# Optimization experiments

Measured on AMD Instinct MI355X. Metric: run time of the kernel, lower is better.

The kernel has to match this reference:

```python
import jax, jax.numpy as jnp
import numpy as np


def setup_inputs() -> dict:
    key = jax.random.key(0)
    ks = jax.random.split(key, 6)
    B, S, F = 8, 2048, 1024
    scale = 1.0 / np.sqrt(F)
    return {
        "query": jax.random.normal(ks[0], (B, S, F), dtype=jnp.float32),
        "key": jax.random.normal(ks[1], (B, S, F), dtype=jnp.float32),
        "value": jax.random.normal(ks[2], (B, S, F), dtype=jnp.float32),
        "Wq": jax.random.normal(ks[3], (F, F), dtype=jnp.float32) * scale,
        "Wk": jax.random.normal(ks[4], (F, F), dtype=jnp.float32) * scale,
        "Wv": jax.random.normal(ks[5], (F, F), dtype=jnp.float32) * scale,
    }


def reference(query, key, value, Wq, Wk, Wv):
    # nn.Linear(bias=False): x @ W.T, W is [out, in]
    q_t = jnp.einsum('bsf,gf->bsg', query, Wq)
    k_t = jnp.einsum('bsf,gf->bsg', key, Wk)
    v_t = jnp.einsum('bsf,gf->bsg', value, Wv)
    F = k_t.shape[-1]
    scale = jnp.asarray(1.0, q_t.dtype) / jnp.sqrt(jnp.asarray(F, q_t.dtype))
    attn = jnp.einsum('bij,bkj->bik', q_t, k_t) * scale  # [B, S, S]
    # original uses nn.Softmax(dim=1): softmax over the query (i) axis
    attn = jax.nn.softmax(attn, axis=1)
    # 'bii,bij->bij': diagonal of attn scales rows of v_t
    diag = jnp.diagonal(attn, axis1=1, axis2=2)  # [B, S]
    proj = diag[:, :, None] * v_t  # [B, S, F]
    return proj
```

## Files before the change

kernel.cpp:

```cpp
#include <hip/hip_runtime.h>


typedef _Float16 f16x8 __attribute__((ext_vector_type(8)));
typedef float    f32x4 __attribute__((ext_vector_type(4)));

#define COLIC 8
#define SCALE 0.03125f

typedef __attribute__((address_space(1))) const unsigned int g_u32_t;
typedef __attribute__((address_space(3))) unsigned int l_u32_t;

__device__ __forceinline__ void gload16(const _Float16* g, _Float16* l) {
  __builtin_amdgcn_global_load_lds((g_u32_t*)g, (l_u32_t*)l, 16, 0, 0);
}

__device__ __forceinline__ void stage_tile64(const _Float16* gbase, int ldk,
                                             _Float16* lds, int w, int lane) {
#pragma unroll
  for (int c = 0; c < 4; ++c) {
    const int blk = c * 4 + w;
    const int o = (blk << 10) + (lane << 4);
    const int row = o >> 7;
    const int colb = (o & 127) ^ ((row & 7) << 4);
    gload16(gbase + (size_t)row * ldk + (colb >> 1), lds + (blk << 9));
  }
}

struct Conv3Args {
  const float* src[3];
  _Float16* dst[3];
};
__global__ __launch_bounds__(256)
void conv3_f32_f16(Conv3Args a, int n8) {
  const float* __restrict__ src = a.src[blockIdx.y];
  _Float16* __restrict__ dst = a.dst[blockIdx.y];
  for (int i = blockIdx.x * 256 + threadIdx.x; i < n8; i += gridDim.x * 256) {
    const float4 x = ((const float4*)src)[2 * i];
    const float4 y = ((const float4*)src)[2 * i + 1];
    f16x8 o;
    o[0] = (_Float16)x.x; o[1] = (_Float16)x.y;
    o[2] = (_Float16)x.z; o[3] = (_Float16)x.w;
    o[4] = (_Float16)y.x; o[5] = (_Float16)y.y;
    o[6] = (_Float16)y.z; o[7] = (_Float16)y.w;
    ((f16x8*)dst)[i] = o;
  }
}

template <int F16OUT>
__global__ __launch_bounds__(256)
void gemm_mfma(const _Float16* __restrict__ A, const _Float16* __restrict__ B,
               _Float16* __restrict__ C16, float* __restrict__ C32,
               const float* __restrict__ mpart, const float* __restrict__ lpart,
               const float* __restrict__ sdiag, int BSz,
               int M, int N, int Kd) {
  __shared__ __align__(16) _Float16 As[128 * 64];
  __shared__ __align__(16) _Float16 Bs[128 * 64];
  __shared__ float diagS[128];
  const int tid = threadIdx.x;
  const int w = tid >> 6, lane = tid & 63;
  const int wr = w >> 1, wc = w & 1;
  const int lr = lane & 15, kq = lane >> 4;
  const int swz = (lr & 7) << 4;
  const int bm = blockIdx.x * 128, bn = blockIdx.y * 128;

  if (!F16OUT && tid < 128) {
    const int row = bm + tid;
    float Mx = -3.0e38f;
#pragma unroll
    for (int c = 0; c < COLIC; ++c) Mx = fmaxf(Mx, mpart[(size_t)c * BSz + row]);
    float L = 0.0f;
#pragma unroll
    for (int c = 0; c < COLIC; ++c)
      L += lpart[(size_t)c * BSz + row] * __expf(mpart[(size_t)c * BSz + row] - Mx);
    diagS[tid] = __expf(sdiag[row] - Mx) / L;
  }

  f32x4 acc[4][4] = {};
  for (int k0 = 0; k0 < Kd; k0 += 64) {
    stage_tile64(A + (size_t)bm * Kd + k0, Kd, As, w, lane);
    stage_tile64(B + (size_t)bn * Kd + k0, Kd, Bs, w, lane);
    __syncthreads();
    f16x8 af[4][2], bf[4][2];
#pragma unroll
    for (int mi = 0; mi < 4; ++mi) {
      const int ro = (wr * 64 + mi * 16 + lr) << 7;
      af[mi][0] = *(const f16x8*)&As[(ro + ((kq * 16) ^ swz)) >> 1];
      af[mi][1] = *(const f16x8*)&As[(ro + ((64 + kq * 16) ^ swz)) >> 1];
    }
#pragma unroll
    for (int ni = 0; ni < 4; ++ni) {
      const int ro = (wc * 64 + ni * 16 + lr) << 7;
      bf[ni][0] = *(const f16x8*)&Bs[(ro + ((kq * 16) ^ swz)) >> 1];
      bf[ni][1] = *(const f16x8*)&Bs[(ro + ((64 + kq * 16) ^ swz)) >> 1];
    }
#pragma unroll
    for (int ks = 0; ks < 2; ++ks)
#pragma unroll
      for (int mi = 0; mi < 4; ++mi)
#pragma unroll
        for (int ni = 0; ni < 4; ++ni)
          acc[mi][ni] = __builtin_amdgcn_mfma_f32_16x16x32_f16(af[mi][ks], bf[ni][ks], acc[mi][ni], 0, 0, 0);
    __syncthreads();
  }
#pragma unroll
  for (int mi = 0; mi < 4; ++mi) {
#pragma unroll
    for (int j = 0; j < 4; ++j) {
      const int rloc = wr * 64 + mi * 16 + kq * 4 + j;
      const int row = bm + rloc;
      float s = 1.0f;
      if (!F16OUT) s = diagS[rloc];
#pragma unroll
      for (int ni = 0; ni < 4; ++ni) {
        const int col = bn + wc * 64 + ni * 16 + lr;
        if (F16OUT) C16[(size_t)row * N + col] = (_Float16)acc[mi][ni][j];
        else        C32[(size_t)row * N + col] = acc[mi][ni][j] * s;
      }
    }
  }
}

__global__ __launch_bounds__(256)
void col_stats_mfma(const _Float16* __restrict__ qt, const _Float16* __restrict__ kt,
                    float* __restrict__ mpart, float* __restrict__ lpart,
                    float* __restrict__ sdiag, int S, int Fd, int chunk) {
  __shared__ __align__(16) _Float16 Qs[128 * 64];
  __shared__ __align__(16) _Float16 Ks[128 * 64];
  __shared__ float redM[8][128];
  __shared__ float redL[8][128];
  const int b = blockIdx.z, jb = blockIdx.x, ic = blockIdx.y;
  const int j0 = jb * 128;
  const _Float16* Q = qt + (size_t)b * S * Fd;
  const _Float16* K = kt + (size_t)b * S * Fd;
  const int tid = threadIdx.x;
  const int w = tid >> 6, lane = tid & 63;
  const int wr = w >> 1, wc = w & 1;
  const int lr = lane & 15, kq = lane >> 4;
  const int swz = (lr & 7) << 4;

  float m[4], l[4];
#pragma unroll
  for (int ni = 0; ni < 4; ++ni) { m[ni] = -3.0e38f; l[ni] = 0.0f; }

  for (int it = 0; it < chunk >> 7; ++it) {
    const int i0 = ic * chunk + (it << 7);
    f32x4 acc[4][4] = {};
    for (int k0 = 0; k0 < Fd; k0 += 64) {
      stage_tile64(Q + (size_t)i0 * Fd + k0, Fd, Qs, w, lane);
      stage_tile64(K + (size_t)j0 * Fd + k0, Fd, Ks, w, lane);
      __syncthreads();
      f16x8 af[4][2], bf[4][2];
#pragma unroll
      for (int mi = 0; mi < 4; ++mi) {
        const int ro = (wr * 64 + mi * 16 + lr) << 7;
        af[mi][0] = *(const f16x8*)&Qs[(ro + ((kq * 16) ^ swz)) >> 1];
        af[mi][1] = *(const f16x8*)&Qs[(ro + ((64 + kq * 16) ^ swz)) >> 1];
      }
#pragma unroll
      for (int ni = 0; ni < 4; ++ni) {
        const int ro = (wc * 64 + ni * 16 + lr) << 7;
        bf[ni][0] = *(const f16x8*)&Ks[(ro + ((kq * 16) ^ swz)) >> 1];
        bf[ni][1] = *(const f16x8*)&Ks[(ro + ((64 + kq * 16) ^ swz)) >> 1];
      }
#pragma unroll
      for (int ks = 0; ks < 2; ++ks)
#pragma unroll
        for (int mi = 0; mi < 4; ++mi)
#pragma unroll
          for (int ni = 0; ni < 4; ++ni)
            acc[mi][ni] = __builtin_amdgcn_mfma_f32_16x16x32_f16(af[mi][ks], bf[ni][ks], acc[mi][ni], 0, 0, 0);
      __syncthreads();
    }
    if (i0 == j0 && wr == wc && (lr >> 2) == kq) {
      const int j = lr & 3;
#pragma unroll
      for (int jj = 0; jj < 4; ++jj)
        sdiag[(size_t)b * S + j0 + wc * 64 + jj * 16 + lr] = acc[jj][jj][j] * SCALE;
    }
#pragma unroll
    for (int ni = 0; ni < 4; ++ni) {
      float tm = -3.0e38f;
#pragma unroll
      for (int mi = 0; mi < 4; ++mi)
#pragma unroll
        for (int jj = 0; jj < 4; ++jj) tm = fmaxf(tm, acc[mi][ni][jj]);
      tm *= SCALE;
      const float mn = fmaxf(m[ni], tm);
      float add = 0.0f;
#pragma unroll
      for (int mi = 0; mi < 4; ++mi)
#pragma unroll
        for (int jj = 0; jj < 4; ++jj) add += __expf(acc[mi][ni][jj] * SCALE - mn);
      l[ni] = l[ni] * __expf(m[ni] - mn) + add;
      m[ni] = mn;
    }
  }
  __syncthreads();
  const int p = wr * 4 + kq;
#pragma unroll
  for (int ni = 0; ni < 4; ++ni) {
    const int col = wc * 64 + ni * 16 + lr;
    redM[p][col] = m[ni];
    redL[p][col] = l[ni];
  }
  __syncthreads();
  if (tid < 128) {
    float M = -3.0e38f;
#pragma unroll
    for (int q = 0; q < 8; ++q) M = fmaxf(M, redM[q][tid]);
    float L = 0.0f;
#pragma unroll
    for (int q = 0; q < 8; ++q) L += redL[q][tid] * __expf(redM[q][tid] - M);
    const size_t idx = ((size_t)ic * gridDim.z + b) * S + j0 + tid;
    mpart[idx] = M;
    lpart[idx] = L;
  }
}

extern "C" void kernel_launch(void* const* d_in, const int* in_sizes, int n_in,
                              void* d_out, int out_size, void* d_ws, size_t ws_size,
                              hipStream_t stream) {
  const float* query = (const float*)d_in[0];
  const float* key   = (const float*)d_in[1];
  const float* value = (const float*)d_in[2];
  const float* Wq    = (const float*)d_in[3];
  const float* Wk    = (const float*)d_in[4];
  const float* Wv    = (const float*)d_in[5];

  const int F = 1024;
  const int BS = in_sizes[0] / F;
  const int B = 8;
  const int S = BS / B;

  _Float16* q16  = (_Float16*)d_ws;
  _Float16* k16  = q16 + (size_t)BS * F;
  _Float16* v16  = k16 + (size_t)BS * F;
  _Float16* wq16 = v16 + (size_t)BS * F;
  _Float16* wk16 = wq16 + (size_t)F * F;
  _Float16* wv16 = wk16 + (size_t)F * F;
  float* mpart = (float*)(wv16 + (size_t)F * F);
  float* lpart = mpart + (size_t)COLIC * BS;
  float* sdiag = lpart + (size_t)COLIC * BS;

  _Float16* qt16 = (_Float16*)d_out;
  _Float16* kt16 = qt16 + (size_t)BS * F;

  const dim3 blk(256);
  const int n8x = BS * F / 8, n8w = F * F / 8;

  Conv3Args ax; ax.src[0] = query; ax.src[1] = key; ax.src[2] = value;
  ax.dst[0] = q16; ax.dst[1] = k16; ax.dst[2] = v16;
  conv3_f32_f16<<<dim3(2048, 3), blk, 0, stream>>>(ax, n8x);

  Conv3Args aw; aw.src[0] = Wq; aw.src[1] = Wk; aw.src[2] = Wv;
  aw.dst[0] = wq16; aw.dst[1] = wk16; aw.dst[2] = wv16;
  conv3_f32_f16<<<dim3(512, 3), blk, 0, stream>>>(aw, n8w);

  const dim3 ggrid(BS / 128, F / 128);
  gemm_mfma<1><<<ggrid, blk, 0, stream>>>(q16, wq16, qt16, (float*)nullptr,
                                          (const float*)nullptr, (const float*)nullptr,
                                          (const float*)nullptr, BS, BS, F, F);
  gemm_mfma<1><<<ggrid, blk, 0, stream>>>(k16, wk16, kt16, (float*)nullptr,
                                          (const float*)nullptr, (const float*)nullptr,
                                          (const float*)nullptr, BS, BS, F, F);

  const dim3 sgrid(S / 128, COLIC, B);
  col_stats_mfma<<<sgrid, blk, 0, stream>>>(qt16, kt16, mpart, lpart, sdiag,
                                            S, F, S / COLIC);

  gemm_mfma<0><<<ggrid, blk, 0, stream>>>(v16, wv16, (_Float16*)nullptr, (float*)d_out,
                                          mpart, lpart, sdiag, BS, BS, F, F);
}
```

Baseline: 281.8 us.

## Fold Wq and Wk into one combined weight to drop the query projection GEMM

Uses the identity q_t·k_tᵀ = query·(Wqᵀ Wk)·keyᵀ. The code transposes Wq and Wk, multiplies them once into a 1024x1024 matrix W2, then projects only the key through W2. col_stats now reads the raw fp16 query directly, which removes one of the two large projection GEMMs. It also remaps col_stats block indices so that neighbouring blocks share inputs for better cache locality. The trade-off is a small extra FxF GEMM plus a transpose kernel, and a different fp16 rounding path through the combined weight that could change accuracy.

```diff
diff --git a/kernel.cpp b/kernel.cpp
--- a/kernel.cpp
+++ b/kernel.cpp
@@ -46,6 +46,43 @@
   }
 }
 
+struct Conv2Args {
+  const float* src[2];
+  _Float16* dst[2];
+};
+__global__ __launch_bounds__(256)
+void convT_f32_f16(Conv2Args a) {
+  __shared__ float Ts[64][65];
+  const float* __restrict__ src = a.src[blockIdx.z];
+  _Float16* __restrict__ dst = a.dst[blockIdx.z];
+  const int g0 = blockIdx.x * 64, f0 = blockIdx.y * 64;
+  const int tid = threadIdx.x;
+  {
+    const int r = tid >> 4;
+    const int c4 = (tid & 15) << 2;
+#pragma unroll
+    for (int p = 0; p < 4; ++p) {
+      const int row = p * 16 + r;
+      const float4 v = *(const float4*)&src[(size_t)(g0 + row) * 1024 + f0 + c4];
+      Ts[row][c4 + 0] = v.x; Ts[row][c4 + 1] = v.y;
+      Ts[row][c4 + 2] = v.z; Ts[row][c4 + 3] = v.w;
+    }
+  }
+  __syncthreads();
+  {
+    const int f = tid >> 3;
+    const int gs = (tid & 7) << 3;
+#pragma unroll
+    for (int p = 0; p < 2; ++p) {
+      const int fr = p * 32 + f;
+      f16x8 v;
+#pragma unroll
+      for (int j = 0; j < 8; ++j) v[j] = (_Float16)Ts[gs + j][fr];
+      *(f16x8*)&dst[(size_t)(f0 + fr) * 1024 + g0 + gs] = v;
+    }
+  }
+}
+
 template <int F16OUT>
 __global__ __launch_bounds__(256)
 void gemm_mfma(const _Float16* __restrict__ A, const _Float16* __restrict__ B,
@@ -128,7 +165,11 @@
   __shared__ __align__(16) _Float16 Ks[128 * 64];
   __shared__ float redM[8][128];
   __shared__ float redL[8][128];
-  const int b = blockIdx.z, jb = blockIdx.x, ic = blockIdx.y;
+  const int t = blockIdx.x + 16 * (blockIdx.y + 8 * blockIdx.z);
+  const int jb = ((t & 7) << 1) | ((t >> 3) & 1);
+  const int rr = t >> 4;
+  const int ic = rr & 7;
+  const int b  = rr >> 3;
   const int j0 = jb * 128;
   const _Float16* Q = qt + (size_t)b * S * Fd;
   const _Float16* K = kt + (size_t)b * S * Fd;
@@ -211,7 +252,7 @@
     float L = 0.0f;
 #pragma unroll
     for (int q = 0; q < 8; ++q) L += redL[q][tid] * __expf(redM[q][tid] - M);
-    const size_t idx = ((size_t)ic * gridDim.z + b) * S + j0 + tid;
+    const size_t idx = ((size_t)ic * 8 + b) * S + j0 + tid;
     mpart[idx] = M;
     lpart[idx] = L;
   }
@@ -232,18 +273,18 @@
   const int B = 8;
   const int S = BS / B;
 
-  _Float16* q16  = (_Float16*)d_ws;
-  _Float16* k16  = q16 + (size_t)BS * F;
-  _Float16* v16  = k16 + (size_t)BS * F;
-  _Float16* wq16 = v16 + (size_t)BS * F;
-  _Float16* wk16 = wq16 + (size_t)F * F;
-  _Float16* wv16 = wk16 + (size_t)F * F;
-  float* mpart = (float*)(wv16 + (size_t)F * F);
+  _Float16* q16   = (_Float16*)d_ws;
+  _Float16* k16   = q16 + (size_t)BS * F;
+  _Float16* v16   = k16 + (size_t)BS * F;
+  _Float16* wqT16 = v16 + (size_t)BS * F;
+  _Float16* wkT16 = wqT16 + (size_t)F * F;
+  _Float16* wv16  = wkT16 + (size_t)F * F;
+  _Float16* W2h   = wv16 + (size_t)F * F;
+  float* mpart = (float*)(W2h + (size_t)F * F);
   float* lpart = mpart + (size_t)COLIC * BS;
   float* sdiag = lpart + (size_t)COLIC * BS;
 
-  _Float16* qt16 = (_Float16*)d_out;
-  _Float16* kt16 = qt16 + (size_t)BS * F;
+  _Float16* kt2 = (_Float16*)d_out;
 
   const dim3 blk(256);
   const int n8x = BS * F / 8, n8w = F * F / 8;
@@ -252,22 +293,26 @@
   ax.dst[0] = q16; ax.dst[1] = k16; ax.dst[2] = v16;
   conv3_f32_f16<<<dim3(2048, 3), blk, 0, stream>>>(ax, n8x);
 
-  Conv3Args aw; aw.src[0] = Wq; aw.src[1] = Wk; aw.src[2] = Wv;
-  aw.dst[0] = wq16; aw.dst[1] = wk16; aw.dst[2] = wv16;
-  conv3_f32_f16<<<dim3(512, 3), blk, 0, stream>>>(aw, n8w);
-
-  const dim3 ggrid(BS / 128, F / 128);
-  gemm_mfma<1><<<ggrid, blk, 0, stream>>>(q16, wq16, qt16, (float*)nullptr,
-                                          (const float*)nullptr, (const float*)nullptr,
-                                          (const float*)nullptr, BS, BS, F, F);
-  gemm_mfma<1><<<ggrid, blk, 0, stream>>>(k16, wk16, kt16, (float*)nullptr,
-                                          (const float*)nullptr, (const float*)nullptr,
-                                          (const float*)nullptr, BS, BS, F, F);
+  Conv3Args av; av.src[0] = Wv; av.dst[0] = wv16;
+  conv3_f32_f16<<<dim3(512, 1), blk, 0, stream>>>(av, n8w);
+
+  Conv2Args at; at.src[0] = Wq; at.src[1] = Wk;
+  at.dst[0] = wqT16; at.dst[1] = wkT16;
+  convT_f32_f16<<<dim3(16, 16, 2), blk, 0, stream>>>(at);
+
+  gemm_mfma<1><<<dim3(8, 8), blk, 0, stream>>>(wqT16, wkT16, W2h, (float*)nullptr,
+                                               (const float*)nullptr, (const float*)nullptr,
+                                               (const float*)nullptr, 0, F, F, F);
+
+  gemm_mfma<1><<<dim3(BS / 128, F / 128), blk, 0, stream>>>(k16, W2h, kt2, (float*)nullptr,
+                                               (const float*)nullptr, (const float*)nullptr,
+                                               (const float*)nullptr, 0, BS, F, F);
 
   const dim3 sgrid(S / 128, COLIC, B);
-  col_stats_mfma<<<sgrid, blk, 0, stream>>>(qt16, kt16, mpart, lpart, sdiag,
+  col_stats_mfma<<<sgrid, blk, 0, stream>>>(q16, kt2, mpart, lpart, sdiag,
                                             S, F, S / COLIC);
 
-  gemm_mfma<0><<<ggrid, blk, 0, stream>>>(v16, wv16, (_Float16*)nullptr, (float*)d_out,
-                                          mpart, lpart, sdiag, BS, BS, F, F);
-}
+  gemm_mfma<0><<<dim3(BS / 128, F / 128), blk, 0, stream>>>(v16, wv16, (_Float16*)nullptr,
+                                               (float*)d_out, mpart, lpart, sdiag,
+                                               BS, BS, F, F);
+}
```

New measurement: 270.8 us. -3.9%, faster.
